# Kernel optimization log

Hardware: AMD Instinct MI355X
Metric: run time of the kernel (lower is better)

The kernel has to match this reference:

```python
import jax, jax.numpy as jnp
import numpy as np


def _gelu(v):
    return jax.nn.gelu(v, approximate=False)


def _conv1x1(x, W, b):
    # x: [B, Ci, H, W], W: [Co, Ci]
    return jnp.einsum('bixy,oi->boxy', x, W) + b[None, :, None, None]


def _spectral(x, w1r, w2r, m1, m2):
    # x: [B, Ci, H, W]; w*r: [Ci, Co, m1, m2, 2] (real/imag)
    w1 = w1r[..., 0] + 1j * w1r[..., 1]
    w2 = w2r[..., 0] + 1j * w2r[..., 1]
    B, C, H, W = x.shape
    xf = jnp.fft.rfft2(x)  # [B, Ci, H, W//2+1] complex64
    o1 = jnp.einsum('bixy,ioxy->boxy', xf[:, :, :m1, :m2], w1)
    o2 = jnp.einsum('bixy,ioxy->boxy', xf[:, :, H - m1:, :m2], w2)
    Co = w1.shape[1]
    of = jnp.zeros((B, Co, H, W // 2 + 1), dtype=xf.dtype)
    of = of.at[:, :, :m1, :m2].set(o1)
    of = of.at[:, :, H - m1:, :m2].set(o2)
    return jnp.fft.irfft2(of, s=(H, W))


def _pool(x):
    B, C, H, W = x.shape
    return x.reshape(B, C, H // 2, 2, W // 2, 2).mean(axis=(3, 5))


def _up(x):
    # matches torch F.interpolate(scale_factor=2, mode='bilinear', align_corners=False)
    B, C, H, W = x.shape
    return jax.image.resize(x, (B, C, 2 * H, 2 * W), method='bilinear')


def _forward(x, fcin_w, fcin_b, sc1_w1, sc1_w2, c1_w, c1_b, sc2_w1, sc2_w2, c2_w, c2_b,
             scb_w1, scb_w2, cb_w, cb_b, su2_w1, su2_w2, u2_w, u2_b,
             su1_w1, su1_w2, u1_w, u1_b, fc1_w, fc1_b, fc2_w, fc2_b):
    v = jnp.einsum('bhwi,oi->bhwo', x, fcin_w) + fcin_b   # lift 6 -> width
    v = v.transpose(0, 3, 1, 2)                            # [B, C, H, W]
    x1 = _gelu(_spectral(v, sc1_w1, sc1_w2, 12, 12) + _conv1x1(v, c1_w, c1_b))
    x1d = _pool(x1)
    x2 = _gelu(_spectral(x1d, sc2_w1, sc2_w2, 8, 8) + _conv1x1(x1d, c2_w, c2_b))
    x2d = _pool(x2)
    xb = _gelu(_spectral(x2d, scb_w1, scb_w2, 4, 4) + _conv1x1(x2d, cb_w, cb_b))
    x2c = jnp.concatenate([_up(xb), x2], axis=1)           # [B, 3.5w, H/2, W/2]
    x2o = _gelu(_spectral(x2c, su2_w1, su2_w2, 8, 8) + _conv1x1(x2c, u2_w, u2_b))
    x1c = jnp.concatenate([_up(x2o), x1], axis=1)          # [B, 2.5w, H, W]
    x1o = _gelu(_spectral(x1c, su1_w1, su1_w2, 12, 12) + _conv1x1(x1c, u1_w, u1_b))
    h = x1o.transpose(0, 2, 3, 1)
    h = _gelu(jnp.einsum('bhwi,oi->bhwo', h, fc1_w) + fc1_b)
    return jnp.einsum('bhwi,oi->bhwo', h, fc2_w) + fc2_b   # [B, H, W, 3]


def setup_inputs() -> dict:
    key = jax.random.key(0)
    ks = jax.random.split(key, 20)

    def cw(k, ci, co, m):  # complex spectral weight stored as [...,2] real
        return (1.0 / (ci * co)) * jax.random.normal(k, (ci, co, m, m, 2), dtype=jnp.float32)

    def lin(k, o, i):
        k1, k2 = jax.random.split(k)
        lim = 1.0 / np.sqrt(i)
        return (jax.random.uniform(k1, (o, i), jnp.float32, -lim, lim),
                jax.random.uniform(k2, (o,), jnp.float32, -lim, lim))

    d = {}
    d['x'] = jax.random.normal(ks[0], (4, 256, 256, 6), dtype=jnp.float32)
    d['fcin_w'], d['fcin_b'] = lin(ks[1], 64, 6)
    d['sc1_w1'] = cw(ks[2], 64, 64, 12); d['sc1_w2'] = cw(ks[3], 64, 64, 12)
    d['c1_w'], d['c1_b'] = lin(ks[4], 64, 64)
    d['sc2_w1'] = cw(ks[5], 64, 96, 8); d['sc2_w2'] = cw(ks[6], 64, 96, 8)
    d['c2_w'], d['c2_b'] = lin(ks[7], 96, 64)
    d['scb_w1'] = cw(ks[8], 96, 128, 4); d['scb_w2'] = cw(ks[9], 96, 128, 4)
    d['cb_w'], d['cb_b'] = lin(ks[10], 128, 96)
    d['su2_w1'] = cw(ks[11], 224, 96, 8); d['su2_w2'] = cw(ks[12], 224, 96, 8)
    d['u2_w'], d['u2_b'] = lin(ks[13], 96, 224)
    d['su1_w1'] = cw(ks[14], 160, 64, 12); d['su1_w2'] = cw(ks[15], 160, 64, 12)
    d['u1_w'], d['u1_b'] = lin(ks[16], 64, 160)
    d['fc1_w'], d['fc1_b'] = lin(ks[17], 256, 64)
    d['fc2_w'], d['fc2_b'] = lin(ks[18], 3, 256)
    return d


def reference(x, fcin_w, fcin_b, sc1_w1, sc1_w2, c1_w, c1_b, sc2_w1, sc2_w2, c2_w, c2_b,
              scb_w1, scb_w2, cb_w, cb_b, su2_w1, su2_w2, u2_w, u2_b,
              su1_w1, su1_w2, u1_w, u1_b, fc1_w, fc1_b, fc2_w, fc2_b):
    return _forward(x, fcin_w, fcin_b, sc1_w1, sc1_w2, c1_w, c1_b, sc2_w1, sc2_w2, c2_w, c2_b,
                    scb_w1, scb_w2, cb_w, cb_b, su2_w1, su2_w2, u2_w, u2_b,
                    su1_w1, su1_w2, u1_w, u1_b, fc1_w, fc1_b, fc2_w, fc2_b)
```

## Files before the change

kernel.cpp:

```cpp
#include <hip/hip_runtime.h>
#include <math.h>
#include <cstdio>


__device__ __forceinline__ float gelu_f(float v) {
    return 0.5f * v * (1.0f + erff(v * 0.70710678118654752f));
}

__global__ __launch_bounds__(256) void init_tw_kernel(float2* tw) {
    int t = threadIdx.x;
    tw[t] = make_float2(cospif(t * (1.0f / 128.0f)), sinpif(t * (1.0f / 128.0f)));
}

__global__ __launch_bounds__(256) void transpose_mat_kernel(const float* __restrict__ src,
                                                            float* __restrict__ dst,
                                                            int Co, int Ci) {
    int idx = blockIdx.x * blockDim.x + threadIdx.x;
    if (idx >= Ci * Co) return;
    int o = idx % Co; int i = idx / Co;
    dst[idx] = src[(size_t)o * Ci + i];
}

template <int M2, int SRC, int W_T>
__global__ __launch_bounds__(256, 4) void dftx_kernel(
    const float* __restrict__ U, int C, int Coff, int Ctot,
    int H, int Hs, int Ws,
    const float* __restrict__ liftW, const float* __restrict__ liftB,
    int stepW, const float2* __restrict__ tw, float2* __restrict__ Fx) {
    constexpr int W = W_T;
    constexpr int WS2 = W_T / 2;
    __shared__ float2 twxk[(SRC == 2) ? (WS2 * M2) : (W * M2)];
    int tid = threadIdx.x;
    if constexpr (SRC == 2) {
        for (int t = tid; t < WS2 * M2; t += 256) {
            int j = t / M2, k = t - (t / M2) * M2;
            float wr = 0.f, wi = 0.f;
            auto addE = [&](int xx, float w) {
                float2 e = tw[(xx * k * stepW) & 255];
                wr += w * e.x; wi += w * e.y;
            };
            if (j == 0)            { addE(0, 1.0f); addE(1, 0.75f); addE(2, 0.25f); }
            else if (j == WS2 - 1) { addE(2 * j - 1, 0.25f); addE(2 * j, 0.75f); addE(2 * j + 1, 1.0f); }
            else                   { addE(2 * j - 1, 0.25f); addE(2 * j, 0.75f);
                                     addE(2 * j + 1, 0.75f); addE(2 * j + 2, 0.25f); }
            twxk[t] = make_float2(wr, wi);
        }
    } else {
        for (int t = tid; t < W * M2; t += 256) {
            int x = t / M2, k = t - (t / M2) * M2;
            twxk[t] = tw[(x * k * stepW) & 255];
        }
    }
    __syncthreads();
    int by = blockIdx.x * 4 + (tid >> 6);
    int c = blockIdx.y * 64 + (tid & 63);
    if (c >= C) return;

    const float* rowD = nullptr;
    const float* Sa = nullptr; const float* Sb = nullptr;
    float wy = 0.f, bc = 0.f;
    float w6[6] = {0, 0, 0, 0, 0, 0};
    if constexpr (SRC == 0) {
        rowD = U + (size_t)by * W * C + c;
    } else if constexpr (SRC == 1) {
        bc = liftB[c];
#pragma unroll
        for (int j = 0; j < 6; j++) w6[j] = liftW[c * 6 + j];
    } else {
        int b = by / H, y = by % H;
        float fy = 0.5f * y - 0.25f;
        int y0 = (int)floorf(fy); wy = fy - y0;
        int ya = y0 < 0 ? 0 : y0;
        int yb = (y0 + 1 > Hs - 1) ? Hs - 1 : y0 + 1;
        Sa = U + ((size_t)(b * Hs + ya) * Ws) * C + c;
        Sb = U + ((size_t)(b * Hs + yb) * Ws) * C + c;
    }

    float ar[M2], ai[M2];
#pragma unroll
    for (int k = 0; k < M2; k++) { ar[k] = 0.f; ai[k] = 0.f; }
    if constexpr (SRC == 2) {
        for (int js = 0; js < WS2; js++) {
            float sa = Sa[(size_t)js * C], sb = Sb[(size_t)js * C];
            float u = sa * (1.f - wy) + sb * wy;
            const float4* gp = (const float4*)&twxk[js * M2];
#pragma unroll
            for (int k2 = 0; k2 < M2 / 2; k2++) {
                float4 g4 = gp[k2];
                ar[2 * k2] += u * g4.x;     ai[2 * k2] -= u * g4.y;
                ar[2 * k2 + 1] += u * g4.z; ai[2 * k2 + 1] -= u * g4.w;
            }
        }
    } else {
        for (int x = 0; x < W; x++) {
            float u;
            if constexpr (SRC == 0) {
                u = rowD[(size_t)x * C];
            } else {
                const float* xp = U + ((size_t)by * W + x) * 6;
                u = bc;
#pragma unroll
                for (int j = 0; j < 6; j++) u += w6[j] * xp[j];
            }
            const float4* wp = (const float4*)&twxk[x * M2];
#pragma unroll
            for (int k2 = 0; k2 < M2 / 2; k2++) {
                float4 t4 = wp[k2];
                ar[2 * k2] += u * t4.x;     ai[2 * k2] -= u * t4.y;
                ar[2 * k2 + 1] += u * t4.z; ai[2 * k2 + 1] -= u * t4.w;
            }
        }
    }
    float2* o = Fx + ((size_t)by * M2) * Ctot + Coff + c;
#pragma unroll
    for (int k = 0; k < M2; k++) o[(size_t)k * Ctot] = make_float2(ar[k], ai[k]);
}

__global__ __launch_bounds__(256, 4) void dfty_kernel(
    const float2* __restrict__ Fx, int H, int m1, int m2, int Ct,
    int stepH, const float2* __restrict__ tw, float2* __restrict__ XF, int N) {
    __shared__ float twc[256], tws[256];
    for (int t = threadIdx.x; t < 256; t += blockDim.x) {
        float2 v = tw[t]; twc[t] = v.x; tws[t] = v.y;
    }
    __syncthreads();
    int idx = blockIdx.x * blockDim.x + threadIdx.x;
    if (idx >= N) return;
    int c = idx % Ct; int r = idx / Ct;
    int kx = r % m2;  r /= m2;
    int kyi = r % (2 * m1); int b = r / (2 * m1);
    int ky = (kyi < m1) ? kyi : (H - 2 * m1 + kyi);
    int tstep = (ky * stepH) & 255;
    const float2* base = Fx + ((size_t)(b * H) * m2 + kx) * Ct + c;
    size_t stride = (size_t)m2 * Ct;
    float accr = 0.f, acci = 0.f;
    int t = 0;
    for (int y = 0; y < H; y++) {
        float2 f = base[(size_t)y * stride];
        float cc = twc[t], ss = tws[t];
        accr += f.x * cc + f.y * ss;
        acci += f.y * cc - f.x * ss;
        t = (t + tstep) & 255;
    }
    XF[idx] = make_float2(accr, acci);
}

__global__ __launch_bounds__(128, 2) void modemix2_kernel(
    const float2* __restrict__ XF,
    const float* __restrict__ w1f, const float* __restrict__ w2f,
    int Ci, int Co, int m1, int m2, float2* __restrict__ OF) {
    __shared__ float2 xsm[4][224];
    int mode = blockIdx.x;
    int nmode = 2 * m1 * m2;
    for (int t = threadIdx.x; t < 4 * Ci; t += blockDim.x) {
        int b = t / Ci, i = t - b * Ci;
        xsm[b][i] = XF[((size_t)b * nmode + mode) * Ci + i];
    }
    __syncthreads();
    int o = threadIdx.x;
    if (o >= Co) return;
    int kx = mode % m2; int kyi = mode / m2;
    const float2* w = (const float2*)((kyi < m1) ? w1f : w2f);
    int ky = (kyi < m1) ? kyi : (kyi - m1);
    float ar0 = 0, ai0 = 0, ar1 = 0, ai1 = 0, ar2 = 0, ai2 = 0, ar3 = 0, ai3 = 0;
    for (int i = 0; i < Ci; i++) {
        float2 wv = w[(((size_t)i * Co + o) * m1 + ky) * m2 + kx];
        float2 a = xsm[0][i], b2 = xsm[1][i], c2 = xsm[2][i], d2 = xsm[3][i];
        ar0 += a.x * wv.x - a.y * wv.y;  ai0 += a.x * wv.y + a.y * wv.x;
        ar1 += b2.x * wv.x - b2.y * wv.y; ai1 += b2.x * wv.y + b2.y * wv.x;
        ar2 += c2.x * wv.x - c2.y * wv.y; ai2 += c2.x * wv.y + c2.y * wv.x;
        ar3 += d2.x * wv.x - d2.y * wv.y; ai3 += d2.x * wv.y + d2.y * wv.x;
    }
    OF[((size_t)0 * nmode + mode) * Co + o] = make_float2(ar0, ai0);
    OF[((size_t)1 * nmode + mode) * Co + o] = make_float2(ar1, ai1);
    OF[((size_t)2 * nmode + mode) * Co + o] = make_float2(ar2, ai2);
    OF[((size_t)3 * nmode + mode) * Co + o] = make_float2(ar3, ai3);
}

__global__ __launch_bounds__(256, 4) void idfty_kernel(
    const float2* __restrict__ OF, int H, int m1, int m2, int Co,
    int stepH, const float2* __restrict__ tw, float2* __restrict__ Gy, int N) {
    __shared__ float twc[256], tws[256];
    for (int t = threadIdx.x; t < 256; t += blockDim.x) {
        float2 v = tw[t]; twc[t] = v.x; tws[t] = v.y;
    }
    __syncthreads();
    int idx = blockIdx.x * blockDim.x + threadIdx.x;
    if (idx >= N) return;
    int o = idx % Co; int r = idx / Co;
    int kx = r % m2;  r /= m2;
    int y = r % H;    int b = r / H;
    float accr = 0.f, acci = 0.f;
    for (int kyi = 0; kyi < 2 * m1; kyi++) {
        int ky = (kyi < m1) ? kyi : (H - 2 * m1 + kyi);
        int t = (ky * y * stepH) & 255;
        float2 f = OF[((size_t)(b * 2 * m1 + kyi) * m2 + kx) * Co + o];
        float cc = twc[t], ss = tws[t];
        accr += f.x * cc - f.y * ss;
        acci += f.x * ss + f.y * cc;
    }
    Gy[idx] = make_float2(accr, acci);
}

template <int SRCA, bool HASB, int CO, int CI, int M2, int MINW>
__global__ __launch_bounds__((CO / 4) * 8, MINW) void synth_kernel(
    const float2* __restrict__ Gy,
    const float* __restrict__ A, int CA, int HsA, int WsA,
    const float* __restrict__ UB, int CB,
    const float* __restrict__ liftW, const float* __restrict__ liftB,
    const float* __restrict__ WcT, const float* __restrict__ bias,
    int H, int W, int stepW, float invHW,
    const float2* __restrict__ tw, float* __restrict__ out) {
    constexpr int OQ = CO / 4;
    constexpr int BLK = OQ * 8;
    constexpr int P = 32;
    constexpr int CIP = CI + 1;
    __shared__ float xs[P][CIP];
    __shared__ float2 twL[M2][P];
    int tid = threadIdx.x;
    int pix0 = blockIdx.x * P;
    int x0 = pix0 % W;  int by = pix0 / W;
    for (int t = tid; t < M2 * P; t += BLK) {
        int k = t / P, p = t - (t / P) * P;
        float2 v = tw[((x0 + p) * k * stepW) & 255];
        float s = ((k == 0) ? 1.f : 2.f) * invHW;
        twL[k][p] = make_float2(s * v.x, s * v.y);
    }
    for (int t = tid; t < P * CI; t += BLK) {
        int p = t / CI, i = t - p * CI;
        int pix = pix0 + p;
        float val;
        if (HASB && i >= CA) {
            val = UB[(size_t)pix * CB + (i - CA)];
        } else if constexpr (SRCA == 0) {
            val = A[(size_t)pix * CA + i];
        } else if constexpr (SRCA == 1) {
            const float* xp = A + (size_t)pix * 6;
            float a = liftB[i];
#pragma unroll
            for (int j = 0; j < 6; j++) a += xp[j] * liftW[i * 6 + j];
            val = a;
        } else {
            int xx = pix % W; int r = pix / W; int y = r % H; int b = r / H;
            float fy = 0.5f * y - 0.25f, fx = 0.5f * xx - 0.25f;
            int y0 = (int)floorf(fy); float wy = fy - y0;
            int x0i = (int)floorf(fx); float wx = fx - x0i;
            int ya = y0 < 0 ? 0 : y0;
            int yb = (y0 + 1 > HsA - 1) ? HsA - 1 : y0 + 1;
            int xa = x0i < 0 ? 0 : x0i;
            int xb2 = (x0i + 1 > WsA - 1) ? WsA - 1 : x0i + 1;
            const float* base = A + ((size_t)b * HsA * WsA) * CA + i;
            float v00 = base[((size_t)ya * WsA + xa) * CA];
            float v01 = base[((size_t)ya * WsA + xb2) * CA];
            float v10 = base[((size_t)yb * WsA + xa) * CA];
            float v11 = base[((size_t)yb * WsA + xb2) * CA];
            val = (1.f - wy) * ((1.f - wx) * v00 + wx * v01) +
                  wy * ((1.f - wx) * v10 + wx * v11);
        }
        xs[p][i] = val;
    }
    __syncthreads();
    int oq = tid % OQ, pg = tid / OQ;
    float acc[4][4];
#pragma unroll
    for (int q = 0; q < 4; q++)
#pragma unroll
        for (int j = 0; j < 4; j++) acc[q][j] = 0.f;
    const float2* grow = Gy + ((size_t)by * M2) * CO + oq * 4;
#pragma unroll
    for (int k = 0; k < M2; k++) {
        float4 ga = *(const float4*)&grow[(size_t)k * CO];
        float4 gb = *(const float4*)&grow[(size_t)k * CO + 2];
#pragma unroll
        for (int q = 0; q < 4; q++) {
            float2 tq = twL[k][pg * 4 + q];
            acc[q][0] += ga.x * tq.x - ga.y * tq.y;
            acc[q][1] += ga.z * tq.x - ga.w * tq.y;
            acc[q][2] += gb.x * tq.x - gb.y * tq.y;
            acc[q][3] += gb.z * tq.x - gb.w * tq.y;
        }
    }
    const float* wrow = WcT + oq * 4;
#pragma unroll 8
    for (int i = 0; i < CI; i++) {
        float4 w = *(const float4*)&wrow[(size_t)i * CO];
#pragma unroll
        for (int q = 0; q < 4; q++) {
            float a = xs[pg * 4 + q][i];
            acc[q][0] += a * w.x; acc[q][1] += a * w.y;
            acc[q][2] += a * w.z; acc[q][3] += a * w.w;
        }
    }
    float4 bb = *(const float4*)&bias[oq * 4];
#pragma unroll
    for (int q = 0; q < 4; q++) {
        int pix = pix0 + pg * 4 + q;
        float4 r;
        r.x = gelu_f(acc[q][0] + bb.x);
        r.y = gelu_f(acc[q][1] + bb.y);
        r.z = gelu_f(acc[q][2] + bb.z);
        r.w = gelu_f(acc[q][3] + bb.w);
        *(float4*)&out[(size_t)pix * CO + oq * 4] = r;
    }
}

__global__ __launch_bounds__(256, 2) void head_kernel(
    const float* __restrict__ xin, const float* __restrict__ fc1t,
    const float* __restrict__ fc1b, const float* __restrict__ fc2w,
    const float* __restrict__ fc2b, float* __restrict__ out) {
    __shared__ float xs[16][65];
    __shared__ float red[64][49];
    int tid = threadIdx.x;
    int pix0 = blockIdx.x * 16;
    const float* src = xin + (size_t)pix0 * 64;
    for (int t = tid; t < 16 * 64; t += 256) xs[t >> 6][t & 63] = src[t];
    __syncthreads();
    int jq = tid & 63, pg = tid >> 6;
    float acc[4][4];
#pragma unroll
    for (int q = 0; q < 4; q++)
#pragma unroll
        for (int j = 0; j < 4; j++) acc[q][j] = 0.f;
    const float* wrow = fc1t + jq * 4;
    for (int i = 0; i < 64; i++) {
        float4 w = *(const float4*)&wrow[(size_t)i * 256];
#pragma unroll
        for (int q = 0; q < 4; q++) {
            float a = xs[pg * 4 + q][i];
            acc[q][0] += a * w.x; acc[q][1] += a * w.y;
            acc[q][2] += a * w.z; acc[q][3] += a * w.w;
        }
    }
    float4 b1 = *(const float4*)&fc1b[jq * 4];
    float4 w20 = *(const float4*)&fc2w[0 * 256 + jq * 4];
    float4 w21 = *(const float4*)&fc2w[1 * 256 + jq * 4];
    float4 w22 = *(const float4*)&fc2w[2 * 256 + jq * 4];
#pragma unroll
    for (int q = 0; q < 4; q++) {
        float h0 = gelu_f(acc[q][0] + b1.x);
        float h1 = gelu_f(acc[q][1] + b1.y);
        float h2 = gelu_f(acc[q][2] + b1.z);
        float h3 = gelu_f(acc[q][3] + b1.w);
        int col = (pg * 4 + q) * 3;
        red[jq][col + 0] = h0 * w20.x + h1 * w20.y + h2 * w20.z + h3 * w20.w;
        red[jq][col + 1] = h0 * w21.x + h1 * w21.y + h2 * w21.z + h3 * w21.w;
        red[jq][col + 2] = h0 * w22.x + h1 * w22.y + h2 * w22.z + h3 * w22.w;
    }
    __syncthreads();
    if (tid < 48) {
        float s = 0.f;
        for (int j = 0; j < 64; j++) s += red[j][tid];
        int px = tid / 3, o3 = tid - 3 * px;
        out[(size_t)(pix0 + px) * 3 + o3] = s + fc2b[o3];
    }
}

__global__ __launch_bounds__(256, 4) void pool_kernel(
    const float* __restrict__ in, float* __restrict__ out,
    int H2, int W2, int C, int N) {
    int idx = blockIdx.x * blockDim.x + threadIdx.x;
    if (idx >= N) return;
    int c = idx % C; int r = idx / C;
    int xo = r % W2; r /= W2;
    int yo = r % H2; int b = r / H2;
    int W = W2 * 2;
    const float* p = in + (((size_t)(b * (H2 * 2) + 2 * yo) * W) + 2 * xo) * C + c;
    float v = p[0] + p[C] + p[(size_t)W * C] + p[(size_t)W * C + C];
    out[idx] = 0.25f * v;
}


static inline unsigned nb_(size_t n, int b) { return (unsigned)((n + b - 1) / b); }

extern "C" void kernel_launch(void* const* d_in, const int* in_sizes, int n_in,
                              void* d_out, int out_size, void* d_ws, size_t ws_size,
                              hipStream_t stream) {
    (void)in_sizes; (void)n_in; (void)out_size;
    const float* x      = (const float*)d_in[0];
    const float* fcin_w = (const float*)d_in[1];
    const float* fcin_b = (const float*)d_in[2];
    const float* sc1_w1 = (const float*)d_in[3];
    const float* sc1_w2 = (const float*)d_in[4];
    const float* c1_w   = (const float*)d_in[5];
    const float* c1_b   = (const float*)d_in[6];
    const float* sc2_w1 = (const float*)d_in[7];
    const float* sc2_w2 = (const float*)d_in[8];
    const float* c2_w   = (const float*)d_in[9];
    const float* c2_b   = (const float*)d_in[10];
    const float* scb_w1 = (const float*)d_in[11];
    const float* scb_w2 = (const float*)d_in[12];
    const float* cb_w   = (const float*)d_in[13];
    const float* cb_b   = (const float*)d_in[14];
    const float* su2_w1 = (const float*)d_in[15];
    const float* su2_w2 = (const float*)d_in[16];
    const float* u2_w   = (const float*)d_in[17];
    const float* u2_b   = (const float*)d_in[18];
    const float* su1_w1 = (const float*)d_in[19];
    const float* su1_w2 = (const float*)d_in[20];
    const float* u1_w   = (const float*)d_in[21];
    const float* u1_b   = (const float*)d_in[22];
    const float* fc1_w  = (const float*)d_in[23];
    const float* fc1_b  = (const float*)d_in[24];
    const float* fc2_w  = (const float*)d_in[25];
    const float* fc2_b  = (const float*)d_in[26];
    float* out = (float*)d_out;

    float* wsf = (float*)d_ws;
    size_t off = 0;
    auto alloc = [&](size_t nfloats) -> float* {
        float* p = wsf + off;
        off += (nfloats + 63) & ~(size_t)63;
        return p;
    };

    float2* tw = (float2*)alloc(512);
    float* c1t  = alloc(64 * 64);
    float* c2t  = alloc(64 * 96);
    float* cbt  = alloc(96 * 128);
    float* u2t  = alloc(224 * 96);
    float* u1t  = alloc(160 * 64);
    float* fc1t = alloc(64 * 256);

    float* x1  = alloc((size_t)4 * 256 * 256 * 64);
    float* x1d = alloc((size_t)4 * 128 * 128 * 64);
    float* x2  = alloc((size_t)4 * 128 * 128 * 96);
    float* xb  = alloc((size_t)4 * 64 * 64 * 128);
    float* x2o = alloc((size_t)4 * 128 * 128 * 96);

    float2* Fx = (float2*)alloc((size_t)2 * 4 * 256 * 12 * 160);
    float2* XF = (float2*)alloc((size_t)2 * 4 * 24 * 12 * 160);
    float2* OF = (float2*)alloc((size_t)2 * 4 * 24 * 12 * 128);
    float2* Gy = (float2*)alloc((size_t)2 * 4 * 256 * 12 * 96);

    size_t need = off * sizeof(float);
    if (ws_size < need) {
        fprintf(stderr, "[FNO2d] workspace too small: need %zu bytes, have %zu\n",
                need, ws_size);
        return;
    }
    float* x2d = x1d;

    init_tw_kernel<<<1, 256, 0, stream>>>(tw);
    transpose_mat_kernel<<<nb_(64 * 64, 256), 256, 0, stream>>>(c1_w, c1t, 64, 64);
    transpose_mat_kernel<<<nb_(64 * 96, 256), 256, 0, stream>>>(c2_w, c2t, 96, 64);
    transpose_mat_kernel<<<nb_(96 * 128, 256), 256, 0, stream>>>(cb_w, cbt, 128, 96);
    transpose_mat_kernel<<<nb_(224 * 96, 256), 256, 0, stream>>>(u2_w, u2t, 96, 224);
    transpose_mat_kernel<<<nb_(160 * 64, 256), 256, 0, stream>>>(u1_w, u1t, 64, 160);
    transpose_mat_kernel<<<nb_(64 * 256, 256), 256, 0, stream>>>(fc1_w, fc1t, 256, 64);

    int N;

    dftx_kernel<12, 1, 256><<<dim3(256, 1), 256, 0, stream>>>(
        x, 64, 0, 64, 256, 0, 0, fcin_w, fcin_b, 1, tw, Fx);
    N = 4 * 24 * 12 * 64;
    dfty_kernel<<<nb_(N, 256), 256, 0, stream>>>(Fx, 256, 12, 12, 64, 1, tw, XF, N);
    modemix2_kernel<<<288, 128, 0, stream>>>(XF, sc1_w1, sc1_w2, 64, 64, 12, 12, OF);
    N = 4 * 256 * 12 * 64;
    idfty_kernel<<<nb_(N, 256), 256, 0, stream>>>(OF, 256, 12, 12, 64, 1, tw, Gy, N);
    synth_kernel<1, false, 64, 64, 12, 3><<<4 * 256 * 256 / 32, 128, 0, stream>>>(
        Gy, x, 64, 0, 0, nullptr, 0, fcin_w, fcin_b, c1t, c1_b,
        256, 256, 1, 1.0f / 65536.0f, tw, x1);
    N = 4 * 128 * 128 * 64;
    pool_kernel<<<nb_(N, 256), 256, 0, stream>>>(x1, x1d, 128, 128, 64, N);

    dftx_kernel<8, 0, 128><<<dim3(128, 1), 256, 0, stream>>>(
        x1d, 64, 0, 64, 128, 0, 0, nullptr, nullptr, 2, tw, Fx);
    N = 4 * 16 * 8 * 64;
    dfty_kernel<<<nb_(N, 256), 256, 0, stream>>>(Fx, 128, 8, 8, 64, 2, tw, XF, N);
    modemix2_kernel<<<128, 128, 0, stream>>>(XF, sc2_w1, sc2_w2, 64, 96, 8, 8, OF);
    N = 4 * 128 * 8 * 96;
    idfty_kernel<<<nb_(N, 256), 256, 0, stream>>>(OF, 128, 8, 8, 96, 2, tw, Gy, N);
    synth_kernel<0, false, 96, 64, 8, 3><<<4 * 128 * 128 / 32, 192, 0, stream>>>(
        Gy, x1d, 64, 0, 0, nullptr, 0, nullptr, nullptr, c2t, c2_b,
        128, 128, 2, 1.0f / 16384.0f, tw, x2);
    N = 4 * 64 * 64 * 96;
    pool_kernel<<<nb_(N, 256), 256, 0, stream>>>(x2, x2d, 64, 64, 96, N);

    dftx_kernel<4, 0, 64><<<dim3(64, 2), 256, 0, stream>>>(
        x2d, 96, 0, 96, 64, 0, 0, nullptr, nullptr, 4, tw, Fx);
    N = 4 * 8 * 4 * 96;
    dfty_kernel<<<nb_(N, 256), 256, 0, stream>>>(Fx, 64, 4, 4, 96, 4, tw, XF, N);
    modemix2_kernel<<<32, 128, 0, stream>>>(XF, scb_w1, scb_w2, 96, 128, 4, 4, OF);
    N = 4 * 64 * 4 * 128;
    idfty_kernel<<<nb_(N, 256), 256, 0, stream>>>(OF, 64, 4, 4, 128, 4, tw, Gy, N);
    synth_kernel<0, false, 128, 96, 4, 2><<<4 * 64 * 64 / 32, 256, 0, stream>>>(
        Gy, x2d, 96, 0, 0, nullptr, 0, nullptr, nullptr, cbt, cb_b,
        64, 64, 4, 1.0f / 4096.0f, tw, xb);

    dftx_kernel<8, 2, 128><<<dim3(128, 2), 256, 0, stream>>>(
        xb, 128, 0, 224, 128, 64, 64, nullptr, nullptr, 2, tw, Fx);
    dftx_kernel<8, 0, 128><<<dim3(128, 2), 256, 0, stream>>>(
        x2, 96, 128, 224, 128, 0, 0, nullptr, nullptr, 2, tw, Fx);
    N = 4 * 16 * 8 * 224;
    dfty_kernel<<<nb_(N, 256), 256, 0, stream>>>(Fx, 128, 8, 8, 224, 2, tw, XF, N);
    modemix2_kernel<<<128, 128, 0, stream>>>(XF, su2_w1, su2_w2, 224, 96, 8, 8, OF);
    N = 4 * 128 * 8 * 96;
    idfty_kernel<<<nb_(N, 256), 256, 0, stream>>>(OF, 128, 8, 8, 96, 2, tw, Gy, N);
    synth_kernel<2, true, 96, 224, 8, 2><<<4 * 128 * 128 / 32, 192, 0, stream>>>(
        Gy, xb, 128, 64, 64, x2, 96, nullptr, nullptr, u2t, u2_b,
        128, 128, 2, 1.0f / 16384.0f, tw, x2o);

    dftx_kernel<12, 2, 256><<<dim3(256, 2), 256, 0, stream>>>(
        x2o, 96, 0, 160, 256, 128, 128, nullptr, nullptr, 1, tw, Fx);
    dftx_kernel<12, 0, 256><<<dim3(256, 1), 256, 0, stream>>>(
        x1, 64, 96, 160, 256, 0, 0, nullptr, nullptr, 1, tw, Fx);
    N = 4 * 24 * 12 * 160;
    dfty_kernel<<<nb_(N, 256), 256, 0, stream>>>(Fx, 256, 12, 12, 160, 1, tw, XF, N);
    modemix2_kernel<<<288, 128, 0, stream>>>(XF, su1_w1, su1_w2, 160, 64, 12, 12, OF);
    N = 4 * 256 * 12 * 64;
    idfty_kernel<<<nb_(N, 256), 256, 0, stream>>>(OF, 256, 12, 12, 64, 1, tw, Gy, N);
    synth_kernel<2, true, 64, 160, 12, 3><<<4 * 256 * 256 / 32, 128, 0, stream>>>(
        Gy, x2o, 96, 128, 128, x1, 64, nullptr, nullptr, u1t, u1_b,
        256, 256, 1, 1.0f / 65536.0f, tw, x1);

    head_kernel<<<4 * 256 * 256 / 16, 256, 0, stream>>>(
        x1, fc1t, fc1_b, fc2_w, fc2_b, out);
}
```

Baseline: 1.671 ms.

## Restructure y-DFT to reuse loads across modes and widen synth register tiles

The y-direction DFT becomes a block-per-(kx, channel tile, batch) kernel. Each thread loads an Fx element once, accumulates it into all 2*M1 ky outputs in registers, and the four y-quarters are reduced through shared memory. Before, every output re-read the whole column. The synth kernel now gives each thread 8 output channels instead of 4 and takes a templated pixel-group count, which cuts redundant shared and weight loads per FMA. The costs are higher register pressure, lower occupancy, and fewer blocks for the small dfty launches.

```diff
diff --git a/kernel.cpp b/kernel.cpp
--- a/kernel.cpp
+++ b/kernel.cpp
@@ -116,33 +116,64 @@
     for (int k = 0; k < M2; k++) o[(size_t)k * Ctot] = make_float2(ar[k], ai[k]);
 }
 
-__global__ __launch_bounds__(256, 4) void dfty_kernel(
-    const float2* __restrict__ Fx, int H, int m1, int m2, int Ct,
-    int stepH, const float2* __restrict__ tw, float2* __restrict__ XF, int N) {
+template <int M1>
+__global__ __launch_bounds__(256, 2) void dfty2_kernel(
+    const float2* __restrict__ Fx, int H, int m2, int Ct,
+    int stepH, const float2* __restrict__ tw, float2* __restrict__ XF) {
+    constexpr int NKY = 2 * M1;
     __shared__ float twc[256], tws[256];
-    for (int t = threadIdx.x; t < 256; t += blockDim.x) {
+    __shared__ float2 red[3][NKY][64];
+    int tid = threadIdx.x;
+    for (int t = tid; t < 256; t += 256) {
         float2 v = tw[t]; twc[t] = v.x; tws[t] = v.y;
     }
     __syncthreads();
-    int idx = blockIdx.x * blockDim.x + threadIdx.x;
-    if (idx >= N) return;
-    int c = idx % Ct; int r = idx / Ct;
-    int kx = r % m2;  r /= m2;
-    int kyi = r % (2 * m1); int b = r / (2 * m1);
-    int ky = (kyi < m1) ? kyi : (H - 2 * m1 + kyi);
-    int tstep = (ky * stepH) & 255;
-    const float2* base = Fx + ((size_t)(b * H) * m2 + kx) * Ct + c;
-    size_t stride = (size_t)m2 * Ct;
-    float accr = 0.f, acci = 0.f;
-    int t = 0;
-    for (int y = 0; y < H; y++) {
-        float2 f = base[(size_t)y * stride];
-        float cc = twc[t], ss = tws[t];
-        accr += f.x * cc + f.y * ss;
-        acci += f.y * cc - f.x * ss;
-        t = (t + tstep) & 255;
-    }
-    XF[idx] = make_float2(accr, acci);
+    int kx = blockIdx.x % m2; int ct = blockIdx.x / m2;
+    int b = blockIdx.y;
+    int lane = tid & 63, grp = tid >> 6;
+    int c = ct * 64 + lane;
+    float ar[NKY], ai[NKY];
+#pragma unroll
+    for (int k = 0; k < NKY; k++) { ar[k] = 0.f; ai[k] = 0.f; }
+    if (c < Ct) {
+        int ylen = H >> 2;
+        int y0 = grp * ylen;
+        const float2* base = Fx + ((size_t)(b * H + y0) * m2 + kx) * Ct + c;
+        size_t stride = (size_t)m2 * Ct;
+        for (int yy = 0; yy < ylen; yy++) {
+            float2 f = base[(size_t)yy * stride];
+            int a = ((y0 + yy) * stepH) & 255;
+            int t = 0;
+#pragma unroll
+            for (int j = 0; j < M1; j++) {
+                float cc = twc[t], ss = tws[t];
+                ar[j] += f.x * cc + f.y * ss;
+                ai[j] += f.y * cc - f.x * ss;
+                t = (t + a) & 255;
+            }
+            t = (M1 * 256 - M1 * a) & 255;
+#pragma unroll
+            for (int j = 0; j < M1; j++) {
+                float cc = twc[t], ss = tws[t];
+                ar[M1 + j] += f.x * cc + f.y * ss;
+                ai[M1 + j] += f.y * cc - f.x * ss;
+                t = (t + a) & 255;
+            }
+        }
+    }
+    if (grp > 0) {
+#pragma unroll
+        for (int k = 0; k < NKY; k++) red[grp - 1][k][lane] = make_float2(ar[k], ai[k]);
+    }
+    __syncthreads();
+    if (grp == 0 && c < Ct) {
+#pragma unroll
+        for (int k = 0; k < NKY; k++) {
+            float2 r0 = red[0][k][lane], r1 = red[1][k][lane], r2 = red[2][k][lane];
+            XF[((size_t)(b * NKY + k) * m2 + kx) * Ct + c] =
+                make_float2(ar[k] + r0.x + r1.x + r2.x, ai[k] + r0.y + r1.y + r2.y);
+        }
+    }
 }
 
 __global__ __launch_bounds__(128, 2) void modemix2_kernel(
@@ -202,8 +233,8 @@
     Gy[idx] = make_float2(accr, acci);
 }
 
-template <int SRCA, bool HASB, int CO, int CI, int M2, int MINW>
-__global__ __launch_bounds__((CO / 4) * 8, MINW) void synth_kernel(
+template <int SRCA, bool HASB, int CO, int CI, int M2, int PG, int MINW>
+__global__ __launch_bounds__((CO / 8) * PG, MINW) void synth_kernel(
     const float2* __restrict__ Gy,
     const float* __restrict__ A, int CA, int HsA, int WsA,
     const float* __restrict__ UB, int CB,
@@ -211,9 +242,9 @@
     const float* __restrict__ WcT, const float* __restrict__ bias,
     int H, int W, int stepW, float invHW,
     const float2* __restrict__ tw, float* __restrict__ out) {
-    constexpr int OQ = CO / 4;
-    constexpr int BLK = OQ * 8;
-    constexpr int P = 32;
+    constexpr int OO = CO / 8;
+    constexpr int BLK = OO * PG;
+    constexpr int P = PG * 4;
     constexpr int CIP = CI + 1;
     __shared__ float xs[P][CIP];
     __shared__ float2 twL[M2][P];
@@ -260,47 +291,62 @@
         xs[p][i] = val;
     }
     __syncthreads();
-    int oq = tid % OQ, pg = tid / OQ;
-    float acc[4][4];
+    int oo = tid % OO, pg = tid / OO;
+    float acc[4][8];
 #pragma unroll
     for (int q = 0; q < 4; q++)
 #pragma unroll
-        for (int j = 0; j < 4; j++) acc[q][j] = 0.f;
-    const float2* grow = Gy + ((size_t)by * M2) * CO + oq * 4;
+        for (int j = 0; j < 8; j++) acc[q][j] = 0.f;
+    const float2* grow = Gy + ((size_t)by * M2) * CO + oo * 8;
 #pragma unroll
     for (int k = 0; k < M2; k++) {
-        float4 ga = *(const float4*)&grow[(size_t)k * CO];
-        float4 gb = *(const float4*)&grow[(size_t)k * CO + 2];
+        float4 g0 = *(const float4*)&grow[(size_t)k * CO + 0];
+        float4 g1 = *(const float4*)&grow[(size_t)k * CO + 2];
+        float4 g2 = *(const float4*)&grow[(size_t)k * CO + 4];
+        float4 g3 = *(const float4*)&grow[(size_t)k * CO + 6];
 #pragma unroll
         for (int q = 0; q < 4; q++) {
             float2 tq = twL[k][pg * 4 + q];
-            acc[q][0] += ga.x * tq.x - ga.y * tq.y;
-            acc[q][1] += ga.z * tq.x - ga.w * tq.y;
-            acc[q][2] += gb.x * tq.x - gb.y * tq.y;
-            acc[q][3] += gb.z * tq.x - gb.w * tq.y;
-        }
-    }
-    const float* wrow = WcT + oq * 4;
-#pragma unroll 8
+            acc[q][0] += g0.x * tq.x - g0.y * tq.y;
+            acc[q][1] += g0.z * tq.x - g0.w * tq.y;
+            acc[q][2] += g1.x * tq.x - g1.y * tq.y;
+            acc[q][3] += g1.z * tq.x - g1.w * tq.y;
+            acc[q][4] += g2.x * tq.x - g2.y * tq.y;
+            acc[q][5] += g2.z * tq.x - g2.w * tq.y;
+            acc[q][6] += g3.x * tq.x - g3.y * tq.y;
+            acc[q][7] += g3.z * tq.x - g3.w * tq.y;
+        }
+    }
+    const float* wrow = WcT + oo * 8;
+#pragma unroll 4
     for (int i = 0; i < CI; i++) {
-        float4 w = *(const float4*)&wrow[(size_t)i * CO];
+        float4 wa = *(const float4*)&wrow[(size_t)i * CO];
+        float4 wb = *(const float4*)&wrow[(size_t)i * CO + 4];
 #pragma unroll
         for (int q = 0; q < 4; q++) {
             float a = xs[pg * 4 + q][i];
-            acc[q][0] += a * w.x; acc[q][1] += a * w.y;
-            acc[q][2] += a * w.z; acc[q][3] += a * w.w;
-        }
-    }
-    float4 bb = *(const float4*)&bias[oq * 4];
+            acc[q][0] += a * wa.x; acc[q][1] += a * wa.y;
+            acc[q][2] += a * wa.z; acc[q][3] += a * wa.w;
+            acc[q][4] += a * wb.x; acc[q][5] += a * wb.y;
+            acc[q][6] += a * wb.z; acc[q][7] += a * wb.w;
+        }
+    }
+    float4 ba = *(const float4*)&bias[oo * 8];
+    float4 bb = *(const float4*)&bias[oo * 8 + 4];
 #pragma unroll
     for (int q = 0; q < 4; q++) {
         int pix = pix0 + pg * 4 + q;
-        float4 r;
-        r.x = gelu_f(acc[q][0] + bb.x);
-        r.y = gelu_f(acc[q][1] + bb.y);
-        r.z = gelu_f(acc[q][2] + bb.z);
-        r.w = gelu_f(acc[q][3] + bb.w);
-        *(float4*)&out[(size_t)pix * CO + oq * 4] = r;
+        float4 r0, r1;
+        r0.x = gelu_f(acc[q][0] + ba.x);
+        r0.y = gelu_f(acc[q][1] + ba.y);
+        r0.z = gelu_f(acc[q][2] + ba.z);
+        r0.w = gelu_f(acc[q][3] + ba.w);
+        r1.x = gelu_f(acc[q][4] + bb.x);
+        r1.y = gelu_f(acc[q][5] + bb.y);
+        r1.z = gelu_f(acc[q][6] + bb.z);
+        r1.w = gelu_f(acc[q][7] + bb.w);
+        *(float4*)&out[(size_t)pix * CO + oo * 8] = r0;
+        *(float4*)&out[(size_t)pix * CO + oo * 8 + 4] = r1;
     }
 }
 
@@ -452,12 +498,11 @@
 
     dftx_kernel<12, 1, 256><<<dim3(256, 1), 256, 0, stream>>>(
         x, 64, 0, 64, 256, 0, 0, fcin_w, fcin_b, 1, tw, Fx);
-    N = 4 * 24 * 12 * 64;
-    dfty_kernel<<<nb_(N, 256), 256, 0, stream>>>(Fx, 256, 12, 12, 64, 1, tw, XF, N);
+    dfty2_kernel<12><<<dim3(12, 4), 256, 0, stream>>>(Fx, 256, 12, 64, 1, tw, XF);
     modemix2_kernel<<<288, 128, 0, stream>>>(XF, sc1_w1, sc1_w2, 64, 64, 12, 12, OF);
     N = 4 * 256 * 12 * 64;
     idfty_kernel<<<nb_(N, 256), 256, 0, stream>>>(OF, 256, 12, 12, 64, 1, tw, Gy, N);
-    synth_kernel<1, false, 64, 64, 12, 3><<<4 * 256 * 256 / 32, 128, 0, stream>>>(
+    synth_kernel<1, false, 64, 64, 12, 16, 3><<<4 * 256 * 256 / 64, 128, 0, stream>>>(
         Gy, x, 64, 0, 0, nullptr, 0, fcin_w, fcin_b, c1t, c1_b,
         256, 256, 1, 1.0f / 65536.0f, tw, x1);
     N = 4 * 128 * 128 * 64;
@@ -465,12 +510,11 @@
 
     dftx_kernel<8, 0, 128><<<dim3(128, 1), 256, 0, stream>>>(
         x1d, 64, 0, 64, 128, 0, 0, nullptr, nullptr, 2, tw, Fx);
-    N = 4 * 16 * 8 * 64;
-    dfty_kernel<<<nb_(N, 256), 256, 0, stream>>>(Fx, 128, 8, 8, 64, 2, tw, XF, N);
+    dfty2_kernel<8><<<dim3(8, 4), 256, 0, stream>>>(Fx, 128, 8, 64, 2, tw, XF);
     modemix2_kernel<<<128, 128, 0, stream>>>(XF, sc2_w1, sc2_w2, 64, 96, 8, 8, OF);
     N = 4 * 128 * 8 * 96;
     idfty_kernel<<<nb_(N, 256), 256, 0, stream>>>(OF, 128, 8, 8, 96, 2, tw, Gy, N);
-    synth_kernel<0, false, 96, 64, 8, 3><<<4 * 128 * 128 / 32, 192, 0, stream>>>(
+    synth_kernel<0, false, 96, 64, 8, 16, 2><<<4 * 128 * 128 / 64, 192, 0, stream>>>(
         Gy, x1d, 64, 0, 0, nullptr, 0, nullptr, nullptr, c2t, c2_b,
         128, 128, 2, 1.0f / 16384.0f, tw, x2);
     N = 4 * 64 * 64 * 96;
@@ -478,12 +522,11 @@
 
     dftx_kernel<4, 0, 64><<<dim3(64, 2), 256, 0, stream>>>(
         x2d, 96, 0, 96, 64, 0, 0, nullptr, nullptr, 4, tw, Fx);
-    N = 4 * 8 * 4 * 96;
-    dfty_kernel<<<nb_(N, 256), 256, 0, stream>>>(Fx, 64, 4, 4, 96, 4, tw, XF, N);
+    dfty2_kernel<4><<<dim3(4 * 2, 4), 256, 0, stream>>>(Fx, 64, 4, 96, 4, tw, XF);
     modemix2_kernel<<<32, 128, 0, stream>>>(XF, scb_w1, scb_w2, 96, 128, 4, 4, OF);
     N = 4 * 64 * 4 * 128;
     idfty_kernel<<<nb_(N, 256), 256, 0, stream>>>(OF, 64, 4, 4, 128, 4, tw, Gy, N);
-    synth_kernel<0, false, 128, 96, 4, 2><<<4 * 64 * 64 / 32, 256, 0, stream>>>(
+    synth_kernel<0, false, 128, 96, 4, 8, 2><<<4 * 64 * 64 / 32, 128, 0, stream>>>(
         Gy, x2d, 96, 0, 0, nullptr, 0, nullptr, nullptr, cbt, cb_b,
         64, 64, 4, 1.0f / 4096.0f, tw, xb);
 
@@ -491,12 +534,11 @@
         xb, 128, 0, 224, 128, 64, 64, nullptr, nullptr, 2, tw, Fx);
     dftx_kernel<8, 0, 128><<<dim3(128, 2), 256, 0, stream>>>(
         x2, 96, 128, 224, 128, 0, 0, nullptr, nullptr, 2, tw, Fx);
-    N = 4 * 16 * 8 * 224;
-    dfty_kernel<<<nb_(N, 256), 256, 0, stream>>>(Fx, 128, 8, 8, 224, 2, tw, XF, N);
+    dfty2_kernel<8><<<dim3(8 * 4, 4), 256, 0, stream>>>(Fx, 128, 8, 224, 2, tw, XF);
     modemix2_kernel<<<128, 128, 0, stream>>>(XF, su2_w1, su2_w2, 224, 96, 8, 8, OF);
     N = 4 * 128 * 8 * 96;
     idfty_kernel<<<nb_(N, 256), 256, 0, stream>>>(OF, 128, 8, 8, 96, 2, tw, Gy, N);
-    synth_kernel<2, true, 96, 224, 8, 2><<<4 * 128 * 128 / 32, 192, 0, stream>>>(
+    synth_kernel<2, true, 96, 224, 8, 16, 2><<<4 * 128 * 128 / 64, 192, 0, stream>>>(
         Gy, xb, 128, 64, 64, x2, 96, nullptr, nullptr, u2t, u2_b,
         128, 128, 2, 1.0f / 16384.0f, tw, x2o);
 
@@ -504,12 +546,11 @@
         x2o, 96, 0, 160, 256, 128, 128, nullptr, nullptr, 1, tw, Fx);
     dftx_kernel<12, 0, 256><<<dim3(256, 1), 256, 0, stream>>>(
         x1, 64, 96, 160, 256, 0, 0, nullptr, nullptr, 1, tw, Fx);
-    N = 4 * 24 * 12 * 160;
-    dfty_kernel<<<nb_(N, 256), 256, 0, stream>>>(Fx, 256, 12, 12, 160, 1, tw, XF, N);
+    dfty2_kernel<12><<<dim3(12 * 3, 4), 256, 0, stream>>>(Fx, 256, 12, 160, 1, tw, XF);
     modemix2_kernel<<<288, 128, 0, stream>>>(XF, su1_w1, su1_w2, 160, 64, 12, 12, OF);
     N = 4 * 256 * 12 * 64;
     idfty_kernel<<<nb_(N, 256), 256, 0, stream>>>(OF, 256, 12, 12, 64, 1, tw, Gy, N);
-    synth_kernel<2, true, 64, 160, 12, 3><<<4 * 256 * 256 / 32, 128, 0, stream>>>(
+    synth_kernel<2, true, 64, 160, 12, 16, 2><<<4 * 256 * 256 / 64, 128, 0, stream>>>(
         Gy, x2o, 96, 128, 128, x1, 64, nullptr, nullptr, u1t, u1_b,
         256, 256, 1, 1.0f / 65536.0f, tw, x1);
 
```

Result: slower. 2.017 ms (+20.7%).
